# Optimization experiments

Hardware: AMD Instinct MI355X
Metric: run time of the kernel (lower is better)

The kernel has to match this reference:

```python
import jax, jax.numpy as jnp
import numpy as np

B, T, D, H, E = 4, 2048, 1024, 2048, 8

def setup_inputs() -> dict:
    key = jax.random.key(0)
    ks = jax.random.split(key, 7)
    s_in = 1.0 / np.sqrt(D)
    s_hid = 1.0 / np.sqrt(H)
    return {
        "x": jax.random.normal(ks[0], (B, T, D), dtype=jnp.float32),
        "Wg": jax.random.uniform(ks[1], (D, E), jnp.float32, -s_in, s_in),
        "bg": jax.random.uniform(ks[2], (E,), jnp.float32, -s_in, s_in),
        "W1": jax.random.uniform(ks[3], (E, D, H), jnp.float32, -s_in, s_in),
        "b1": jax.random.uniform(ks[4], (E, H), jnp.float32, -s_in, s_in),
        "W2": jax.random.uniform(ks[5], (E, H, D), jnp.float32, -s_hid, s_hid),
        "b2": jax.random.uniform(ks[6], (E, D), jnp.float32, -s_hid, s_hid),
    }

def reference(x, Wg, bg, W1, b1, W2, b2):
    # gating: [B,T,E]
    gate = jax.nn.softmax(jnp.einsum('btd,de->bte', x, Wg) + bg, axis=-1)
    # all experts densely: hidden [B,T,E,H]
    h = jax.nn.relu(jnp.einsum('btd,edh->bteh', x, W1) + b1)
    # expert outputs [B,T,E,D]
    eo = jnp.einsum('bteh,ehd->bted', h, W2) + b2
    # softmax-weighted sum over experts -> [B,T,D]
    return jnp.einsum('bte,bted->btd', gate, eo)
```

## Files before the change

### kernel.cpp

```cpp
#include <hip/hip_runtime.h>
#include <hip/hip_bf16.h>
#include <stdint.h>


typedef __bf16 bf16_t;
typedef bf16_t bf16x8 __attribute__((ext_vector_type(8)));
typedef bf16_t bf16x4 __attribute__((ext_vector_type(4)));
typedef float  f32x4  __attribute__((ext_vector_type(4)));

#define Ddim 1024
#define Hdim 2048
#define Edim 8
#define Mdim 8192

__device__ __forceinline__ void async16(const void* g, const void* l) {
  __builtin_amdgcn_global_load_lds(
      (const __attribute__((address_space(1))) void*)(uintptr_t)g,
      (__attribute__((address_space(3))) void*)(uint32_t)(uintptr_t)l,
      16, 0, 0);
}

__global__ void gating_kernel(const float* __restrict__ x,
                              const float* __restrict__ Wg,
                              const float* __restrict__ bg,
                              float* __restrict__ gate) {
  const int lane = threadIdx.x & 63;
  const int wid  = threadIdx.x >> 6;
  const int t    = blockIdx.x * 4 + wid;
  const float* xr = x + (size_t)t * Ddim;
  float acc[8] = {0.f,0.f,0.f,0.f,0.f,0.f,0.f,0.f};
  for (int i = lane; i < Ddim; i += 64) {
    float xv = xr[i];
    f32x4 a = *(const f32x4*)(Wg + (size_t)i * 8);
    f32x4 b = *(const f32x4*)(Wg + (size_t)i * 8 + 4);
    acc[0] += xv * a[0]; acc[1] += xv * a[1];
    acc[2] += xv * a[2]; acc[3] += xv * a[3];
    acc[4] += xv * b[0]; acc[5] += xv * b[1];
    acc[6] += xv * b[2]; acc[7] += xv * b[3];
  }
  #pragma unroll
  for (int e = 0; e < 8; ++e) {
    #pragma unroll
    for (int off = 32; off; off >>= 1)
      acc[e] += __shfl_xor(acc[e], off, 64);
  }
  if (lane == 0) {
    float l[8], mx = -1e30f;
    #pragma unroll
    for (int e = 0; e < 8; ++e) { l[e] = acc[e] + bg[e]; mx = fmaxf(mx, l[e]); }
    float s = 0.f;
    #pragma unroll
    for (int e = 0; e < 8; ++e) { l[e] = __expf(l[e] - mx); s += l[e]; }
    float inv = 1.f / s;
    #pragma unroll
    for (int e = 0; e < 8; ++e) gate[(size_t)t * 8 + e] = l[e] * inv;
  }
}

__global__ void cvt_x(const float* __restrict__ a, bf16_t* __restrict__ o) {
  const size_t i = ((size_t)blockIdx.x * 256 + threadIdx.x) * 8;
  f32x4 v0 = *(const f32x4*)(a + i);
  f32x4 v1 = *(const f32x4*)(a + i + 4);
  bf16x8 b;
  b[0]=(bf16_t)v0[0]; b[1]=(bf16_t)v0[1]; b[2]=(bf16_t)v0[2]; b[3]=(bf16_t)v0[3];
  b[4]=(bf16_t)v1[0]; b[5]=(bf16_t)v1[1]; b[6]=(bf16_t)v1[2]; b[7]=(bf16_t)v1[3];
  *(bf16x8*)(o + i) = b;
}

__global__ void transpose_f32_bf16(const float* __restrict__ src,
                                   bf16_t* __restrict__ dst, int R, int C) {
  __shared__ bf16_t tile[32][33];
  const size_t zo = (size_t)blockIdx.z * (size_t)R * C;
  src += zo; dst += zo;
  const int r0 = blockIdx.y * 32, c0 = blockIdx.x * 32;
  const int tr = threadIdx.x >> 3;
  const int tc = (threadIdx.x & 7) * 4;
  f32x4 v = *(const f32x4*)(src + (size_t)(r0 + tr) * C + c0 + tc);
  tile[tr][tc+0] = (bf16_t)v[0]; tile[tr][tc+1] = (bf16_t)v[1];
  tile[tr][tc+2] = (bf16_t)v[2]; tile[tr][tc+3] = (bf16_t)v[3];
  __syncthreads();
  bf16x4 o;
  o[0] = tile[tc+0][tr]; o[1] = tile[tc+1][tr];
  o[2] = tile[tc+2][tr]; o[3] = tile[tc+3][tr];
  *(bf16x4*)(dst + (size_t)(c0 + tr) * R + r0 + tc) = o;
}

__launch_bounds__(256, 2)
__global__ void gemm1_kernel(const bf16_t* __restrict__ A,
                             const bf16_t* __restrict__ W1tAll,
                             const float*  __restrict__ gate,
                             const float*  __restrict__ b1,
                             bf16_t* __restrict__ hgAll,
                             int e0) {
  __shared__ alignas(16) bf16_t sA[128 * 32];
  __shared__ alignas(16) bf16_t sB[128 * 32];

  const int tid  = threadIdx.x;
  const int lane = tid & 63;
  const int wid  = tid >> 6;
  const int wm   = wid >> 1, wn = wid & 1;
  const int lrow = lane & 15, quad = lane >> 4;

  const int z = blockIdx.z;
  const int e = e0 + z;
  const bf16_t* Bt = W1tAll + (size_t)z * Hdim * Ddim;
  bf16_t* hg = hgAll + (size_t)z * Mdim * Hdim;
  const float* bias = b1 + (size_t)e * Hdim;

  const int bid = blockIdx.y * 16 + blockIdx.x;
  const int xcd = bid & 7;
  const int loc = bid >> 3;
  const int tileM = (xcd * 8 + (loc >> 4)) * 128;
  const int tileN = (loc & 15) * 128;

  const int lb0 = tid * 16;
  const int lb1 = 4096 + tid * 16;
  const int r0 = lb0 >> 6, kb0 = lb0 & 63;
  const int r1 = lb1 >> 6, kb1 = lb1 & 63;

  const char* ap0 = (const char*)(A  + (size_t)(tileM + r0) * Ddim) + kb0;
  const char* ap1 = (const char*)(A  + (size_t)(tileM + r1) * Ddim) + kb1;
  const char* bp0 = (const char*)(Bt + (size_t)(tileN + r0) * Ddim) + kb0;
  const char* bp1 = (const char*)(Bt + (size_t)(tileN + r1) * Ddim) + kb1;
  const char* la0  = (const char*)sA + lb0;
  const char* la1  = (const char*)sA + lb1;
  const char* lbp0 = (const char*)sB + lb0;
  const char* lbp1 = (const char*)sB + lb1;

  f32x4 acc[4][4] = {};

  for (int it = 0; it < (Ddim >> 5); ++it) {
    __syncthreads();
    async16(ap0, la0);
    async16(ap1, la1);
    async16(bp0, lbp0);
    async16(bp1, lbp1);
    ap0 += 64; ap1 += 64; bp0 += 64; bp1 += 64;
    __syncthreads();

    bf16x8 af[4], bfr[4];
    #pragma unroll
    for (int i = 0; i < 4; ++i)
      af[i] = *(const bf16x8*)&sA[(wm * 64 + i * 16 + lrow) * 32 + quad * 8];
    #pragma unroll
    for (int j = 0; j < 4; ++j)
      bfr[j] = *(const bf16x8*)&sB[(wn * 64 + j * 16 + lrow) * 32 + quad * 8];
    #pragma unroll
    for (int i = 0; i < 4; ++i)
      #pragma unroll
      for (int j = 0; j < 4; ++j)
        acc[i][j] = __builtin_amdgcn_mfma_f32_16x16x32_bf16(af[i], bfr[j], acc[i][j], 0, 0, 0);
  }

  float bcol[4];
  #pragma unroll
  for (int j = 0; j < 4; ++j)
    bcol[j] = bias[tileN + wn * 64 + j * 16 + lrow];

  #pragma unroll
  for (int i = 0; i < 4; ++i) {
    #pragma unroll
    for (int r = 0; r < 4; ++r) {
      const int row = tileM + wm * 64 + i * 16 + quad * 4 + r;
      const float g = gate[(size_t)row * 8 + e];
      #pragma unroll
      for (int j = 0; j < 4; ++j) {
        const int col = tileN + wn * 64 + j * 16 + lrow;
        float v = acc[i][j][r] + bcol[j];
        v = fmaxf(v, 0.f) * g;
        hg[(size_t)row * Hdim + col] = (bf16_t)v;
      }
    }
  }
}

template <int G, bool FIRST>
__launch_bounds__(256, 2)
__global__ void gemm2_kernel(const bf16_t* __restrict__ hgAll,
                             const bf16_t* __restrict__ W2tAll,
                             const float*  __restrict__ gate,
                             const float*  __restrict__ b2,
                             float* __restrict__ out,
                             int e0) {
  __shared__ alignas(16) bf16_t sA[128 * 32];
  __shared__ alignas(16) bf16_t sB[128 * 32];

  const int tid  = threadIdx.x;
  const int lane = tid & 63;
  const int wid  = tid >> 6;
  const int wm   = wid >> 1, wn = wid & 1;
  const int lrow = lane & 15, quad = lane >> 4;

  const int bid = blockIdx.y * 8 + blockIdx.x;
  const int xcd = bid & 7;
  const int loc = bid >> 3;
  const int tileM = (xcd * 8 + (loc >> 3)) * 128;
  const int tileN = (loc & 7) * 128;

  const int lb0 = tid * 16;
  const int lb1 = 4096 + tid * 16;
  const int r0 = lb0 >> 6, kb0 = lb0 & 63;
  const int r1 = lb1 >> 6, kb1 = lb1 & 63;

  const char* la0  = (const char*)sA + lb0;
  const char* la1  = (const char*)sA + lb1;
  const char* lbp0 = (const char*)sB + lb0;
  const char* lbp1 = (const char*)sB + lb1;

  f32x4 acc[4][4] = {};

  #pragma unroll
  for (int g = 0; g < G; ++g) {
    const bf16_t* Ag = hgAll  + (size_t)g * Mdim * Hdim;
    const bf16_t* Bg = W2tAll + (size_t)g * Ddim * Hdim;
    const char* ap0 = (const char*)(Ag + (size_t)(tileM + r0) * Hdim) + kb0;
    const char* ap1 = (const char*)(Ag + (size_t)(tileM + r1) * Hdim) + kb1;
    const char* bp0 = (const char*)(Bg + (size_t)(tileN + r0) * Hdim) + kb0;
    const char* bp1 = (const char*)(Bg + (size_t)(tileN + r1) * Hdim) + kb1;

    for (int it = 0; it < (Hdim >> 5); ++it) {
      __syncthreads();
      async16(ap0, la0);
      async16(ap1, la1);
      async16(bp0, lbp0);
      async16(bp1, lbp1);
      ap0 += 64; ap1 += 64; bp0 += 64; bp1 += 64;
      __syncthreads();

      bf16x8 af[4], bfr[4];
      #pragma unroll
      for (int i = 0; i < 4; ++i)
        af[i] = *(const bf16x8*)&sA[(wm * 64 + i * 16 + lrow) * 32 + quad * 8];
      #pragma unroll
      for (int j = 0; j < 4; ++j)
        bfr[j] = *(const bf16x8*)&sB[(wn * 64 + j * 16 + lrow) * 32 + quad * 8];
      #pragma unroll
      for (int i = 0; i < 4; ++i)
        #pragma unroll
        for (int j = 0; j < 4; ++j)
          acc[i][j] = __builtin_amdgcn_mfma_f32_16x16x32_bf16(af[i], bfr[j], acc[i][j], 0, 0, 0);
    }
  }

  float b2c[4][G];
  #pragma unroll
  for (int j = 0; j < 4; ++j) {
    const int col = tileN + wn * 64 + j * 16 + lrow;
    #pragma unroll
    for (int g = 0; g < G; ++g)
      b2c[j][g] = b2[(size_t)(e0 + g) * Ddim + col];
  }

  #pragma unroll
  for (int i = 0; i < 4; ++i) {
    #pragma unroll
    for (int r = 0; r < 4; ++r) {
      const int row = tileM + wm * 64 + i * 16 + quad * 4 + r;
      const float* gr = gate + (size_t)row * 8 + e0;
      float gv[G];
      #pragma unroll
      for (int g = 0; g < G; ++g) gv[g] = gr[g];
      #pragma unroll
      for (int j = 0; j < 4; ++j) {
        const int col = tileN + wn * 64 + j * 16 + lrow;
        float v = acc[i][j][r];
        #pragma unroll
        for (int g = 0; g < G; ++g) v += gv[g] * b2c[j][g];
        if (FIRST) out[(size_t)row * Ddim + col] = v;
        else       out[(size_t)row * Ddim + col] += v;
      }
    }
  }
}

extern "C" void kernel_launch(void* const* d_in, const int* in_sizes, int n_in,
                              void* d_out, int out_size, void* d_ws, size_t ws_size,
                              hipStream_t stream) {
  const float* x  = (const float*)d_in[0];
  const float* Wg = (const float*)d_in[1];
  const float* bg = (const float*)d_in[2];
  const float* W1 = (const float*)d_in[3];
  const float* b1 = (const float*)d_in[4];
  const float* W2 = (const float*)d_in[5];
  const float* b2 = (const float*)d_in[6];
  float* out = (float*)d_out;

  int G = 1;
  if      (ws_size >= (size_t)(17 + 40 * 8) << 20) G = 8;
  else if (ws_size >= (size_t)(17 + 40 * 4) << 20) G = 4;
  else if (ws_size >= (size_t)(17 + 40 * 2) << 20) G = 2;

  char* ws = (char*)d_ws;
  float*  gate = (float*)ws;
  bf16_t* xb   = (bf16_t*)(ws + (1u << 20));
  bf16_t* W1t  = (bf16_t*)(ws + (17u << 20));
  bf16_t* W2t  = (bf16_t*)(ws + ((size_t)(17 + 4 * G) << 20));
  bf16_t* hg   = (bf16_t*)(ws + ((size_t)(17 + 8 * G) << 20));

  gating_kernel<<<Mdim / 4, 256, 0, stream>>>(x, Wg, bg, gate);
  cvt_x<<<(Mdim * Ddim) / (256 * 8), 256, 0, stream>>>(x, xb);

  const int nGroups = Edim / G;
  for (int gi = 0; gi < nGroups; ++gi) {
    const int e0 = gi * G;
    transpose_f32_bf16<<<dim3(Hdim / 32, Ddim / 32, G), 256, 0, stream>>>(
        W1 + (size_t)e0 * Ddim * Hdim, W1t, Ddim, Hdim);
    transpose_f32_bf16<<<dim3(Ddim / 32, Hdim / 32, G), 256, 0, stream>>>(
        W2 + (size_t)e0 * Hdim * Ddim, W2t, Hdim, Ddim);

    gemm1_kernel<<<dim3(Hdim / 128, Mdim / 128, G), 256, 0, stream>>>(
        xb, W1t, gate, b1, hg, e0);

    const dim3 g2(Ddim / 128, Mdim / 128);
    const bool first = (gi == 0);
    if (G == 8)      gemm2_kernel<8, true ><<<g2, 256, 0, stream>>>(hg, W2t, gate, b2, out, e0);
    else if (G == 4) {
      if (first)     gemm2_kernel<4, true ><<<g2, 256, 0, stream>>>(hg, W2t, gate, b2, out, e0);
      else           gemm2_kernel<4, false><<<g2, 256, 0, stream>>>(hg, W2t, gate, b2, out, e0);
    } else if (G == 2) {
      if (first)     gemm2_kernel<2, true ><<<g2, 256, 0, stream>>>(hg, W2t, gate, b2, out, e0);
      else           gemm2_kernel<2, false><<<g2, 256, 0, stream>>>(hg, W2t, gate, b2, out, e0);
    } else {
      if (first)     gemm2_kernel<1, true ><<<g2, 256, 0, stream>>>(hg, W2t, gate, b2, out, e0);
      else           gemm2_kernel<1, false><<<g2, 256, 0, stream>>>(hg, W2t, gate, b2, out, e0);
    }
  }
}
```

Before: 862.6 us.

## Rewrite expert GEMMs with 256-tile double-buffered swizzled LDS pipeline

```diff
diff --git a/kernel.cpp b/kernel.cpp
--- a/kernel.cpp
+++ b/kernel.cpp
@@ -19,6 +19,17 @@
       (__attribute__((address_space(3))) void*)(uint32_t)(uintptr_t)l,
       16, 0, 0);
 }
+
+#define MFMA(a, b, c) __builtin_amdgcn_mfma_f32_16x16x32_bf16((a), (b), (c), 0, 0, 0)
+
+#define WAIT_LGKM0() do {                                  \
+    asm volatile("s_waitcnt lgkmcnt(0)" ::: "memory");     \
+    __builtin_amdgcn_sched_barrier(0);                     \
+  } while (0)
+#define WAIT_VM(n) do {                                    \
+    asm volatile("s_waitcnt vmcnt(" #n ")" ::: "memory");  \
+    __builtin_amdgcn_sched_barrier(0);                     \
+  } while (0)
 
 __global__ void gating_kernel(const float* __restrict__ x,
                               const float* __restrict__ Wg,
@@ -85,189 +96,324 @@
   *(bf16x4*)(dst + (size_t)(c0 + tr) * R + r0 + tc) = o;
 }
 
-__launch_bounds__(256, 2)
+__launch_bounds__(512, 2)
 __global__ void gemm1_kernel(const bf16_t* __restrict__ A,
                              const bf16_t* __restrict__ W1tAll,
                              const float*  __restrict__ gate,
                              const float*  __restrict__ b1,
                              bf16_t* __restrict__ hgAll,
                              int e0) {
-  __shared__ alignas(16) bf16_t sA[128 * 32];
-  __shared__ alignas(16) bf16_t sB[128 * 32];
+  __shared__ alignas(16) bf16_t sA[2][256 * 64];
+  __shared__ alignas(16) bf16_t sB[2][256 * 64];
 
   const int tid  = threadIdx.x;
   const int lane = tid & 63;
   const int wid  = tid >> 6;
-  const int wm   = wid >> 1, wn = wid & 1;
+  const int wm   = wid >> 2, wn = wid & 3;
   const int lrow = lane & 15, quad = lane >> 4;
+  const int sb   = quad ^ (lrow & 7);
 
   const int z = blockIdx.z;
   const int e = e0 + z;
   const bf16_t* Bt = W1tAll + (size_t)z * Hdim * Ddim;
-  bf16_t* hg = hgAll + (size_t)z * Mdim * Hdim;
+  bf16_t* hg = hgAll + (size_t)z * (size_t)Mdim * Hdim;
   const float* bias = b1 + (size_t)e * Hdim;
 
-  const int bid = blockIdx.y * 16 + blockIdx.x;
-  const int xcd = bid & 7;
-  const int loc = bid >> 3;
-  const int tileM = (xcd * 8 + (loc >> 4)) * 128;
-  const int tileN = (loc & 15) * 128;
-
-  const int lb0 = tid * 16;
-  const int lb1 = 4096 + tid * 16;
-  const int r0 = lb0 >> 6, kb0 = lb0 & 63;
-  const int r1 = lb1 >> 6, kb1 = lb1 & 63;
-
-  const char* ap0 = (const char*)(A  + (size_t)(tileM + r0) * Ddim) + kb0;
-  const char* ap1 = (const char*)(A  + (size_t)(tileM + r1) * Ddim) + kb1;
-  const char* bp0 = (const char*)(Bt + (size_t)(tileN + r0) * Ddim) + kb0;
-  const char* bp1 = (const char*)(Bt + (size_t)(tileN + r1) * Ddim) + kb1;
-  const char* la0  = (const char*)sA + lb0;
-  const char* la1  = (const char*)sA + lb1;
-  const char* lbp0 = (const char*)sB + lb0;
-  const char* lbp1 = (const char*)sB + lb1;
-
-  f32x4 acc[4][4] = {};
-
-  for (int it = 0; it < (Ddim >> 5); ++it) {
-    __syncthreads();
-    async16(ap0, la0);
-    async16(ap1, la1);
-    async16(bp0, lbp0);
-    async16(bp1, lbp1);
-    ap0 += 64; ap1 += 64; bp0 += 64; bp1 += 64;
-    __syncthreads();
-
-    bf16x8 af[4], bfr[4];
-    #pragma unroll
-    for (int i = 0; i < 4; ++i)
-      af[i] = *(const bf16x8*)&sA[(wm * 64 + i * 16 + lrow) * 32 + quad * 8];
-    #pragma unroll
-    for (int j = 0; j < 4; ++j)
-      bfr[j] = *(const bf16x8*)&sB[(wn * 64 + j * 16 + lrow) * 32 + quad * 8];
-    #pragma unroll
-    for (int i = 0; i < 4; ++i)
-      #pragma unroll
-      for (int j = 0; j < 4; ++j)
-        acc[i][j] = __builtin_amdgcn_mfma_f32_16x16x32_bf16(af[i], bfr[j], acc[i][j], 0, 0, 0);
-  }
-
+  const int bid = blockIdx.y * 8 + blockIdx.x;
+  const int xcd = bid & 7, loc = bid >> 3;
+  const int tileM = (xcd * 4 + (loc >> 3)) * 256;
+  const int tileN = (loc & 7) * 256;
+
+  const int trow = tid >> 3;
+  const int tsw  = ((tid & 7) ^ (trow & 7)) << 4;
+  const int ldst = tid << 4;
+  const size_t SA = (size_t)64 * Ddim * 2;
+
+  const char* a0 = (const char*)(A  + (size_t)(tileM + trow) * Ddim) + tsw;
+  const char* b0 = (const char*)(Bt + (size_t)(tileN + trow) * Ddim) + tsw;
+  char* curA = (char*)&sA[0][0]; char* nxtA = (char*)&sA[1][0];
+  char* curB = (char*)&sB[0][0]; char* nxtB = (char*)&sB[1][0];
+
+  async16(a0,          curA + 0 * 8192 + ldst);
+  async16(a0 + 2 * SA, curA + 2 * 8192 + ldst);
+  async16(b0,          curB + 0 * 8192 + ldst);
+  async16(b0 + SA,     curB + 1 * 8192 + ldst);
+  async16(b0 + 2 * SA, curB + 2 * 8192 + ldst);
+  async16(b0 + 3 * SA, curB + 3 * 8192 + ldst);
+  async16(a0 + SA,     curA + 1 * 8192 + ldst);
+  async16(a0 + 3 * SA, curA + 3 * 8192 + ldst);
+  a0 += 128; b0 += 128;
+  WAIT_VM(0);
+  __builtin_amdgcn_s_barrier();
+
+  f32x4 acc[8][4] = {};
+  const int offA0 = (wm * 128 + lrow) * 128 + sb * 16;
+  const int offA1 = (wm * 128 + lrow) * 128 + (sb ^ 4) * 16;
+  const int offB0 = (wn * 64  + lrow) * 128 + sb * 16;
+  const int offB1 = (wn * 64  + lrow) * 128 + (sb ^ 4) * 16;
+
+  #pragma unroll 1
+  for (int kk = 0; kk < Ddim / 64; ++kk) {
+    const bool notlast = (kk + 1 < Ddim / 64);
+    bf16x8 afr[4][2], bfr[4][2];
+
+    #pragma unroll
+    for (int i = 0; i < 4; ++i) {
+      afr[i][0] = *(const bf16x8*)(curA + offA0 + i * 2048);
+      afr[i][1] = *(const bf16x8*)(curA + offA1 + i * 2048);
+    }
+    #pragma unroll
+    for (int j = 0; j < 2; ++j) {
+      bfr[j][0] = *(const bf16x8*)(curB + offB0 + j * 2048);
+      bfr[j][1] = *(const bf16x8*)(curB + offB1 + j * 2048);
+    }
+    if (notlast) {
+      async16(a0,          nxtA + 0 * 8192 + ldst);
+      async16(a0 + 2 * SA, nxtA + 2 * 8192 + ldst);
+    }
+    __builtin_amdgcn_s_barrier();
+    WAIT_LGKM0();
+    __builtin_amdgcn_s_setprio(1);
+    #pragma unroll
+    for (int i = 0; i < 4; ++i)
+      #pragma unroll
+      for (int j = 0; j < 2; ++j) {
+        acc[i][j] = MFMA(afr[i][0], bfr[j][0], acc[i][j]);
+        acc[i][j] = MFMA(afr[i][1], bfr[j][1], acc[i][j]);
+      }
+    __builtin_amdgcn_s_setprio(0);
+    __builtin_amdgcn_s_barrier();
+
+    #pragma unroll
+    for (int j = 0; j < 2; ++j) {
+      bfr[2 + j][0] = *(const bf16x8*)(curB + offB0 + (2 + j) * 2048);
+      bfr[2 + j][1] = *(const bf16x8*)(curB + offB1 + (2 + j) * 2048);
+    }
+    if (notlast) {
+      async16(b0,          nxtB + 0 * 8192 + ldst);
+      async16(b0 + SA,     nxtB + 1 * 8192 + ldst);
+      async16(b0 + 2 * SA, nxtB + 2 * 8192 + ldst);
+      async16(b0 + 3 * SA, nxtB + 3 * 8192 + ldst);
+    }
+    __builtin_amdgcn_s_barrier();
+    WAIT_LGKM0();
+    __builtin_amdgcn_s_setprio(1);
+    #pragma unroll
+    for (int i = 0; i < 4; ++i)
+      #pragma unroll
+      for (int j = 0; j < 2; ++j) {
+        acc[i][2 + j] = MFMA(afr[i][0], bfr[2 + j][0], acc[i][2 + j]);
+        acc[i][2 + j] = MFMA(afr[i][1], bfr[2 + j][1], acc[i][2 + j]);
+      }
+    __builtin_amdgcn_s_setprio(0);
+    if (notlast) { WAIT_VM(6); } else { WAIT_VM(0); }
+    __builtin_amdgcn_s_barrier();
+
+    #pragma unroll
+    for (int i = 0; i < 4; ++i) {
+      afr[i][0] = *(const bf16x8*)(curA + offA0 + 8192 + i * 2048);
+      afr[i][1] = *(const bf16x8*)(curA + offA1 + 8192 + i * 2048);
+    }
+    if (notlast) {
+      async16(a0 + SA,     nxtA + 1 * 8192 + ldst);
+      async16(a0 + 3 * SA, nxtA + 3 * 8192 + ldst);
+    }
+    __builtin_amdgcn_s_barrier();
+    WAIT_LGKM0();
+    __builtin_amdgcn_s_setprio(1);
+    #pragma unroll
+    for (int i = 0; i < 4; ++i)
+      #pragma unroll
+      for (int j = 0; j < 2; ++j) {
+        acc[4 + i][j] = MFMA(afr[i][0], bfr[j][0], acc[4 + i][j]);
+        acc[4 + i][j] = MFMA(afr[i][1], bfr[j][1], acc[4 + i][j]);
+      }
+    __builtin_amdgcn_s_setprio(0);
+    __builtin_amdgcn_s_barrier();
+
+    __builtin_amdgcn_s_setprio(1);
+    #pragma unroll
+    for (int i = 0; i < 4; ++i)
+      #pragma unroll
+      for (int j = 0; j < 2; ++j) {
+        acc[4 + i][2 + j] = MFMA(afr[i][0], bfr[2 + j][0], acc[4 + i][2 + j]);
+        acc[4 + i][2 + j] = MFMA(afr[i][1], bfr[2 + j][1], acc[4 + i][2 + j]);
+      }
+    __builtin_amdgcn_s_setprio(0);
+    if (notlast) { WAIT_VM(2); } else { WAIT_VM(0); }
+    __builtin_amdgcn_s_barrier();
+
+    a0 += 128; b0 += 128;
+    char* t;
+    t = curA; curA = nxtA; nxtA = t;
+    t = curB; curB = nxtB; nxtB = t;
+  }
+
+  const int col0 = tileN + wn * 64 + lrow;
   float bcol[4];
   #pragma unroll
-  for (int j = 0; j < 4; ++j)
-    bcol[j] = bias[tileN + wn * 64 + j * 16 + lrow];
-
+  for (int j = 0; j < 4; ++j) bcol[j] = bias[col0 + j * 16];
   #pragma unroll
-  for (int i = 0; i < 4; ++i) {
+  for (int i = 0; i < 8; ++i) {
     #pragma unroll
     for (int r = 0; r < 4; ++r) {
-      const int row = tileM + wm * 64 + i * 16 + quad * 4 + r;
+      const int row = tileM + wm * 128 + i * 16 + quad * 4 + r;
       const float g = gate[(size_t)row * 8 + e];
       #pragma unroll
       for (int j = 0; j < 4; ++j) {
-        const int col = tileN + wn * 64 + j * 16 + lrow;
         float v = acc[i][j][r] + bcol[j];
         v = fmaxf(v, 0.f) * g;
-        hg[(size_t)row * Hdim + col] = (bf16_t)v;
+        hg[(size_t)row * Hdim + col0 + j * 16] = (bf16_t)v;
       }
     }
   }
 }
 
 template <int G, bool FIRST>
-__launch_bounds__(256, 2)
+__launch_bounds__(512, 2)
 __global__ void gemm2_kernel(const bf16_t* __restrict__ hgAll,
                              const bf16_t* __restrict__ W2tAll,
                              const float*  __restrict__ gate,
                              const float*  __restrict__ b2,
                              float* __restrict__ out,
                              int e0) {
-  __shared__ alignas(16) bf16_t sA[128 * 32];
-  __shared__ alignas(16) bf16_t sB[128 * 32];
+  __shared__ alignas(16) bf16_t sA[2][256 * 64];
+  __shared__ alignas(16) bf16_t sB[2][128 * 64];
 
   const int tid  = threadIdx.x;
   const int lane = tid & 63;
   const int wid  = tid >> 6;
-  const int wm   = wid >> 1, wn = wid & 1;
+  const int wm   = wid >> 2, wn = wid & 3;
   const int lrow = lane & 15, quad = lane >> 4;
+  const int sb   = quad ^ (lrow & 7);
 
   const int bid = blockIdx.y * 8 + blockIdx.x;
-  const int xcd = bid & 7;
-  const int loc = bid >> 3;
-  const int tileM = (xcd * 8 + (loc >> 3)) * 128;
+  const int xcd = bid & 7, loc = bid >> 3;
+  const int tileM = (xcd * 4 + (loc >> 3)) * 256;
   const int tileN = (loc & 7) * 128;
 
-  const int lb0 = tid * 16;
-  const int lb1 = 4096 + tid * 16;
-  const int r0 = lb0 >> 6, kb0 = lb0 & 63;
-  const int r1 = lb1 >> 6, kb1 = lb1 & 63;
-
-  const char* la0  = (const char*)sA + lb0;
-  const char* la1  = (const char*)sA + lb1;
-  const char* lbp0 = (const char*)sB + lb0;
-  const char* lbp1 = (const char*)sB + lb1;
-
-  f32x4 acc[4][4] = {};
-
+  const int trow = tid >> 3;
+  const int tsw  = ((tid & 7) ^ (trow & 7)) << 4;
+  const int ldst = tid << 4;
+  const size_t S = (size_t)64 * Hdim * 2;
+
+  const char* a0 = (const char*)(hgAll  + (size_t)(tileM + trow) * Hdim) + tsw;
+  const char* b0 = (const char*)(W2tAll + (size_t)(tileN + trow) * Hdim) + tsw;
+  char* curA = (char*)&sA[0][0]; char* nxtA = (char*)&sA[1][0];
+  char* curB = (char*)&sB[0][0]; char* nxtB = (char*)&sB[1][0];
+
+  async16(a0,         curA + 0 * 8192 + ldst);
+  async16(a0 + 2 * S, curA + 2 * 8192 + ldst);
+  async16(b0,         curB + 0 * 8192 + ldst);
+  async16(b0 + S,     curB + 1 * 8192 + ldst);
+  async16(a0 + S,     curA + 1 * 8192 + ldst);
+  async16(a0 + 3 * S, curA + 3 * 8192 + ldst);
+  a0 += 128; b0 += 128;
+  WAIT_VM(0);
+  __builtin_amdgcn_s_barrier();
+
+  f32x4 acc[8][2] = {};
+  const int offA0 = (wm * 128 + lrow) * 128 + sb * 16;
+  const int offA1 = (wm * 128 + lrow) * 128 + (sb ^ 4) * 16;
+  const int offB0 = (wn * 32  + lrow) * 128 + sb * 16;
+  const int offB1 = (wn * 32  + lrow) * 128 + (sb ^ 4) * 16;
+
+  const int NKT = G * (Hdim / 64);
+  #pragma unroll 1
+  for (int kk = 0; kk < NKT; ++kk) {
+    const bool notlast = (kk + 1 < NKT);
+    if (notlast && (((kk + 1) & 31) == 0)) {
+      const int gn = (kk + 1) >> 5;
+      a0 = (const char*)(hgAll  + (size_t)gn * Mdim * Hdim
+                         + (size_t)(tileM + trow) * Hdim) + tsw;
+      b0 = (const char*)(W2tAll + (size_t)gn * Ddim * Hdim
+                         + (size_t)(tileN + trow) * Hdim) + tsw;
+    }
+    bf16x8 afr[4][2], bfr[2][2];
+
+    #pragma unroll
+    for (int i = 0; i < 4; ++i) {
+      afr[i][0] = *(const bf16x8*)(curA + offA0 + i * 2048);
+      afr[i][1] = *(const bf16x8*)(curA + offA1 + i * 2048);
+    }
+    #pragma unroll
+    for (int j = 0; j < 2; ++j) {
+      bfr[j][0] = *(const bf16x8*)(curB + offB0 + j * 2048);
+      bfr[j][1] = *(const bf16x8*)(curB + offB1 + j * 2048);
+    }
+    if (notlast) {
+      async16(a0,         nxtA + 0 * 8192 + ldst);
+      async16(a0 + 2 * S, nxtA + 2 * 8192 + ldst);
+      async16(b0,         nxtB + 0 * 8192 + ldst);
+      async16(b0 + S,     nxtB + 1 * 8192 + ldst);
+    }
+    __builtin_amdgcn_s_barrier();
+    WAIT_LGKM0();
+    __builtin_amdgcn_s_setprio(1);
+    #pragma unroll
+    for (int i = 0; i < 4; ++i)
+      #pragma unroll
+      for (int j = 0; j < 2; ++j) {
+        acc[i][j] = MFMA(afr[i][0], bfr[j][0], acc[i][j]);
+        acc[i][j] = MFMA(afr[i][1], bfr[j][1], acc[i][j]);
+      }
+    __builtin_amdgcn_s_setprio(0);
+    if (notlast) { WAIT_VM(4); } else { WAIT_VM(0); }
+    __builtin_amdgcn_s_barrier();
+
+    #pragma unroll
+    for (int i = 0; i < 4; ++i) {
+      afr[i][0] = *(const bf16x8*)(curA + offA0 + 8192 + i * 2048);
+      afr[i][1] = *(const bf16x8*)(curA + offA1 + 8192 + i * 2048);
+    }
+    if (notlast) {
+      async16(a0 + S,     nxtA + 1 * 8192 + ldst);
+      async16(a0 + 3 * S, nxtA + 3 * 8192 + ldst);
+    }
+    __builtin_amdgcn_s_barrier();
+    WAIT_LGKM0();
+    __builtin_amdgcn_s_setprio(1);
+    #pragma unroll
+    for (int i = 0; i < 4; ++i)
+      #pragma unroll
+      for (int j = 0; j < 2; ++j) {
+        acc[4 + i][j] = MFMA(afr[i][0], bfr[j][0], acc[4 + i][j]);
+        acc[4 + i][j] = MFMA(afr[i][1], bfr[j][1], acc[4 + i][j]);
+      }
+    __builtin_amdgcn_s_setprio(0);
+    if (notlast) { WAIT_VM(2); } else { WAIT_VM(0); }
+    __builtin_amdgcn_s_barrier();
+
+    a0 += 128; b0 += 128;
+    char* t;
+    t = curA; curA = nxtA; nxtA = t;
+    t = curB; curB = nxtB; nxtB = t;
+  }
+
+  const int col0 = tileN + wn * 32 + lrow;
+  float b2c[2][G];
   #pragma unroll
-  for (int g = 0; g < G; ++g) {
-    const bf16_t* Ag = hgAll  + (size_t)g * Mdim * Hdim;
-    const bf16_t* Bg = W2tAll + (size_t)g * Ddim * Hdim;
-    const char* ap0 = (const char*)(Ag + (size_t)(tileM + r0) * Hdim) + kb0;
-    const char* ap1 = (const char*)(Ag + (size_t)(tileM + r1) * Hdim) + kb1;
-    const char* bp0 = (const char*)(Bg + (size_t)(tileN + r0) * Hdim) + kb0;
-    const char* bp1 = (const char*)(Bg + (size_t)(tileN + r1) * Hdim) + kb1;
-
-    for (int it = 0; it < (Hdim >> 5); ++it) {
-      __syncthreads();
-      async16(ap0, la0);
-      async16(ap1, la1);
-      async16(bp0, lbp0);
-      async16(bp1, lbp1);
-      ap0 += 64; ap1 += 64; bp0 += 64; bp1 += 64;
-      __syncthreads();
-
-      bf16x8 af[4], bfr[4];
-      #pragma unroll
-      for (int i = 0; i < 4; ++i)
-        af[i] = *(const bf16x8*)&sA[(wm * 64 + i * 16 + lrow) * 32 + quad * 8];
-      #pragma unroll
-      for (int j = 0; j < 4; ++j)
-        bfr[j] = *(const bf16x8*)&sB[(wn * 64 + j * 16 + lrow) * 32 + quad * 8];
-      #pragma unroll
-      for (int i = 0; i < 4; ++i)
-        #pragma unroll
-        for (int j = 0; j < 4; ++j)
-          acc[i][j] = __builtin_amdgcn_mfma_f32_16x16x32_bf16(af[i], bfr[j], acc[i][j], 0, 0, 0);
-    }
-  }
-
-  float b2c[4][G];
+  for (int j = 0; j < 2; ++j)
+    #pragma unroll
+    for (int g = 0; g < G; ++g)
+      b2c[j][g] = b2[(size_t)(e0 + g) * Ddim + col0 + j * 16];
+
   #pragma unroll
-  for (int j = 0; j < 4; ++j) {
-    const int col = tileN + wn * 64 + j * 16 + lrow;
-    #pragma unroll
-    for (int g = 0; g < G; ++g)
-      b2c[j][g] = b2[(size_t)(e0 + g) * Ddim + col];
-  }
-
-  #pragma unroll
-  for (int i = 0; i < 4; ++i) {
+  for (int i = 0; i < 8; ++i) {
     #pragma unroll
     for (int r = 0; r < 4; ++r) {
-      const int row = tileM + wm * 64 + i * 16 + quad * 4 + r;
+      const int row = tileM + wm * 128 + i * 16 + quad * 4 + r;
       const float* gr = gate + (size_t)row * 8 + e0;
       float gv[G];
       #pragma unroll
       for (int g = 0; g < G; ++g) gv[g] = gr[g];
       #pragma unroll
-      for (int j = 0; j < 4; ++j) {
-        const int col = tileN + wn * 64 + j * 16 + lrow;
+      for (int j = 0; j < 2; ++j) {
         float v = acc[i][j][r];
         #pragma unroll
         for (int g = 0; g < G; ++g) v += gv[g] * b2c[j][g];
-        if (FIRST) out[(size_t)row * Ddim + col] = v;
-        else       out[(size_t)row * Ddim + col] += v;
+        if (FIRST) out[(size_t)row * Ddim + col0 + j * 16] = v;
+        else       out[(size_t)row * Ddim + col0 + j * 16] += v;
       }
     }
   }
@@ -308,21 +454,21 @@
     transpose_f32_bf16<<<dim3(Ddim / 32, Hdim / 32, G), 256, 0, stream>>>(
         W2 + (size_t)e0 * Hdim * Ddim, W2t, Hdim, Ddim);
 
-    gemm1_kernel<<<dim3(Hdim / 128, Mdim / 128, G), 256, 0, stream>>>(
+    gemm1_kernel<<<dim3(Hdim / 256, Mdim / 256, G), 512, 0, stream>>>(
         xb, W1t, gate, b1, hg, e0);
 
-    const dim3 g2(Ddim / 128, Mdim / 128);
+    const dim3 g2(Ddim / 128, Mdim / 256);
     const bool first = (gi == 0);
-    if (G == 8)      gemm2_kernel<8, true ><<<g2, 256, 0, stream>>>(hg, W2t, gate, b2, out, e0);
+    if (G == 8)      gemm2_kernel<8, true ><<<g2, 512, 0, stream>>>(hg, W2t, gate, b2, out, e0);
     else if (G == 4) {
-      if (first)     gemm2_kernel<4, true ><<<g2, 256, 0, stream>>>(hg, W2t, gate, b2, out, e0);
-      else           gemm2_kernel<4, false><<<g2, 256, 0, stream>>>(hg, W2t, gate, b2, out, e0);
+      if (first)     gemm2_kernel<4, true ><<<g2, 512, 0, stream>>>(hg, W2t, gate, b2, out, e0);
+      else           gemm2_kernel<4, false><<<g2, 512, 0, stream>>>(hg, W2t, gate, b2, out, e0);
     } else if (G == 2) {
-      if (first)     gemm2_kernel<2, true ><<<g2, 256, 0, stream>>>(hg, W2t, gate, b2, out, e0);
-      else           gemm2_kernel<2, false><<<g2, 256, 0, stream>>>(hg, W2t, gate, b2, out, e0);
+      if (first)     gemm2_kernel<2, true ><<<g2, 512, 0, stream>>>(hg, W2t, gate, b2, out, e0);
+      else           gemm2_kernel<2, false><<<g2, 512, 0, stream>>>(hg, W2t, gate, b2, out, e0);
     } else {
-      if (first)     gemm2_kernel<1, true ><<<g2, 256, 0, stream>>>(hg, W2t, gate, b2, out, e0);
-      else           gemm2_kernel<1, false><<<g2, 256, 0, stream>>>(hg, W2t, gate, b2, out, e0);
-    }
-  }
-}
+      if (first)     gemm2_kernel<1, true ><<<g2, 512, 0, stream>>>(hg, W2t, gate, b2, out, e0);
+      else           gemm2_kernel<1, false><<<g2, 512, 0, stream>>>(hg, W2t, gate, b2, out, e0);
+    }
+  }
+}
```

Measured after the change: 764.7 us. 1.13x faster.
